# Optimization experiments

Hardware: AMD Instinct MI355X
Metric: run time of the kernel (lower is better)

Reference implementation:

```python
import jax, jax.numpy as jnp
from jax import lax
import numpy as np

B = 2; C = 128; H = 128; W = 128; NPIX = H * W
HTH = 184; HTW = 180; NBINS = HTH * HTW
NSPH = 16384; KHT = 8; KSPH = 16
N0, N1, N2 = 1024, 256, 64
K0, K1, K2 = 8, 8, 8
EPS = 1e-5


def setup_inputs() -> dict:
    key = jax.random.key(0)
    ks = jax.random.split(key, 24)
    f32 = jnp.float32
    inp = {}
    inp["image"] = jax.random.normal(ks[0], (B, C, H, W), f32)
    inp["bn_gamma"] = jnp.ones((C,), f32)
    inp["bn_beta"] = jnp.zeros((C,), f32)
    inp["ht_idx"] = jax.random.randint(ks[1], (NBINS, KHT), 0, NPIX, jnp.int32)
    inp["ht_w"] = jax.random.uniform(ks[2], (NBINS, KHT), f32)
    inp["w_htconv"] = jax.random.normal(ks[3], (3, 3, C, C), f32) / np.sqrt(9.0 * C)
    inp["htbn_gamma"] = jnp.ones((C,), f32)
    inp["htbn_beta"] = jnp.zeros((C,), f32)
    inp["sph_idx"] = jax.random.randint(ks[4], (NSPH, KSPH), 0, NBINS, jnp.int32)
    inp["sph_w"] = jax.random.uniform(ks[5], (NSPH, KSPH), f32)
    inp["w_sc"] = jax.random.normal(ks[6], (3, 64, C), f32) / np.sqrt(1.0 * C)
    inp["b_sc"] = jnp.zeros((3, 64), f32)
    inp["scbn_gamma"] = jnp.ones((3, 64), f32)
    inp["scbn_beta"] = jnp.zeros((3, 64), f32)
    inp["dgcn_w"] = jax.random.normal(ks[7], (3, 4, 128, 64), f32) / np.sqrt(128.0)
    inp["dgcn_b"] = jnp.zeros((3, 4, 64), f32)
    inp["dgcn_hw"] = jax.random.normal(ks[8], (3, 64), f32) / 8.0
    inp["dgcn_hb"] = jnp.zeros((3,), f32)
    inp["ind0"] = jax.random.randint(ks[9], (B, N0), 0, NSPH, jnp.int32)
    inp["ind1"] = jax.random.randint(ks[10], (B, 3, N1), 0, NSPH, jnp.int32)
    inp["ind2"] = jax.random.randint(ks[11], (B, 3, N2), 0, NSPH, jnp.int32)
    # kNN-style edges: structured centers (each node repeated k times), random neighbors
    c0 = jnp.tile(jnp.repeat(jnp.arange(N0, dtype=jnp.int32), K0)[None], (B, 1))
    inp["edge0"] = jnp.stack([c0, jax.random.randint(ks[12], (B, N0 * K0), 0, N0, jnp.int32)], 1)
    c1 = jnp.broadcast_to(jnp.repeat(jnp.arange(N1, dtype=jnp.int32), K1)[None, None], (B, 3, N1 * K1))
    inp["edge1"] = jnp.stack([c1, jax.random.randint(ks[13], (B, 3, N1 * K1), 0, N1, jnp.int32)], 2)
    c2 = jnp.broadcast_to(jnp.repeat(jnp.arange(N2, dtype=jnp.int32), K2)[None, None], (B, 3, N2 * K2))
    inp["edge2"] = jnp.stack([c2, jax.random.randint(ks[14], (B, 3, N2 * K2), 0, N2, jnp.int32)], 2)
    inp["target0"] = jax.random.randint(ks[15], (B, N0), 0, 2, jnp.int32)
    inp["target1"] = jax.random.randint(ks[16], (B * 3, N1), 0, 2, jnp.int32)
    inp["target2"] = jax.random.randint(ks[17], (B * 3, N2), 0, 2, jnp.int32)
    return inp


def _bn2d(x, g, b):
    m = x.mean((0, 2, 3), keepdims=True)
    v = x.var((0, 2, 3), keepdims=True)
    return g[None, :, None, None] * (x - m) * lax.rsqrt(v + EPS) + b[None, :, None, None]


def _sphere(x_htf, sph_idx, sph_w, ind):
    # x_htf: [B,C,NBINS]; ind: [B,S] -> weighted gather of HT bins per sphere node
    mi = sph_idx[ind]          # [B,S,K]
    mw = sph_w[ind]            # [B,S,K]
    g = jax.vmap(lambda xb, ib: xb[:, ib])(x_htf, mi)   # [B,C,S,K]
    return (g * mw[:, None]).sum(-1)                    # [B,C,S]


def _sconv(x, w, b, g, be):
    # 1x1 conv [B,C,S]->[B,64,S] + BN1d (batch stats) + ReLU
    y = jnp.einsum('oc,bcs->bos', w, x) + b[None, :, None]
    m = y.mean((0, 2), keepdims=True)
    v = y.var((0, 2), keepdims=True)
    return jax.nn.relu(g[None, :, None] * (y - m) * lax.rsqrt(v + EPS) + be[None, :, None])


def _dgcn(x, edge, ws, bs, hw, hb, n, k):
    # x: [Bg,n,64]; edge: [Bg,2,n*k] (row0=center, row1=neighbor); 4 EdgeConv layers
    for i in range(4):
        xc = jnp.take_along_axis(x, edge[:, 0, :, None], axis=1)   # [Bg,n*k,Cin]
        xn = jnp.take_along_axis(x, edge[:, 1, :, None], axis=1)
        h = jax.nn.relu(jnp.concatenate([xc, xn - xc], -1) @ ws[i] + bs[i])
        x = h.reshape(x.shape[0], n, k, -1).max(2)                 # max over neighbors
    return x @ hw + hb                                             # [Bg,n] logits


def _bce(logits, target):
    t = target.astype(logits.dtype)
    l = jnp.maximum(logits, 0.0) - logits * t + jnp.log1p(jnp.exp(-jnp.abs(logits)))
    pos = t > 0.5
    npos = jnp.maximum(pos.sum(), 1).astype(l.dtype)
    nneg = jnp.maximum((~pos).sum(), 1).astype(l.dtype)
    return jnp.where(pos, l, 0.0).sum() / npos, jnp.where(pos, 0.0, l).sum() / nneg


def _forward(image, bn_gamma, bn_beta, ht_idx, ht_w, w_htconv, htbn_gamma, htbn_beta,
             sph_idx, sph_w, w_sc, b_sc, scbn_gamma, scbn_beta,
             dgcn_w, dgcn_b, dgcn_hw, dgcn_hb,
             ind0, ind1, ind2, edge0, edge1, edge2, target0, target1, target2):
    x = jax.nn.relu(_bn2d(image, bn_gamma, bn_beta))
    xf = x.reshape(B, C, NPIX)
    # Hough voting: each HT bin accumulates KHT weighted pixels
    ht = (xf[:, :, ht_idx] * ht_w).sum(-1).reshape(B, C, HTH, HTW)
    hc = lax.conv_general_dilated(ht, w_htconv, (1, 1), 'SAME',
                                  dimension_numbers=('NCHW', 'HWIO', 'NCHW'))
    x_htf = jax.nn.relu(_bn2d(hc, htbn_gamma, htbn_beta)).reshape(B, C, NBINS)

    # scale 0
    x0 = _sconv(_sphere(x_htf, sph_idx, sph_w, ind0),
                w_sc[0], b_sc[0], scbn_gamma[0], scbn_beta[0]).transpose(0, 2, 1)
    x0 = _dgcn(x0, edge0, dgcn_w[0], dgcn_b[0], dgcn_hw[0], dgcn_hb[0], N0, K0)   # [B,N0]
    # scale 1 (3 vanishing-point branches folded into batch)
    x1 = _sconv(_sphere(x_htf, sph_idx, sph_w, ind1.reshape(B, -1)),
                w_sc[1], b_sc[1], scbn_gamma[1], scbn_beta[1]).transpose(0, 2, 1)
    x1 = _dgcn(x1.reshape(B * 3, N1, 64), edge1.reshape(B * 3, 2, N1 * K1),
               dgcn_w[1], dgcn_b[1], dgcn_hw[1], dgcn_hb[1], N1, K1)              # [B*3,N1]
    # scale 2
    x2 = _sconv(_sphere(x_htf, sph_idx, sph_w, ind2.reshape(B, -1)),
                w_sc[2], b_sc[2], scbn_gamma[2], scbn_beta[2]).transpose(0, 2, 1)
    x2 = _dgcn(x2.reshape(B * 3, N2, 64), edge2.reshape(B * 3, 2, N2 * K2),
               dgcn_w[2], dgcn_b[2], dgcn_hw[2], dgcn_hb[2], N2, K2)              # [B*3,N2]

    lp0, ln0 = _bce(x0, target0)
    lp1, ln1 = _bce(x1, target1)
    lp2, ln2 = _bce(x2, target2)
    losses = jnp.stack([lp0, ln0, lp1, ln1, lp2, ln2])
    preds = jnp.concatenate([jax.nn.sigmoid(x0).reshape(B, -1),
                             jax.nn.sigmoid(x1).reshape(B, -1),
                             jax.nn.sigmoid(x2).reshape(B, -1)], axis=1)
    return losses, preds


def reference(image, bn_gamma, bn_beta, ht_idx, ht_w, w_htconv, htbn_gamma, htbn_beta,
              sph_idx, sph_w, w_sc, b_sc, scbn_gamma, scbn_beta,
              dgcn_w, dgcn_b, dgcn_hw, dgcn_hb,
              ind0, ind1, ind2, edge0, edge1, edge2, target0, target1, target2):
    return _forward(image, bn_gamma, bn_beta, ht_idx, ht_w, w_htconv, htbn_gamma, htbn_beta,
                    sph_idx, sph_w, w_sc, b_sc, scbn_gamma, scbn_beta,
                    dgcn_w, dgcn_b, dgcn_hw, dgcn_hb,
                    ind0, ind1, ind2, edge0, edge1, edge2, target0, target1, target2)
```

## Files before the change

kernel.cpp:

```cpp
#include <hip/hip_runtime.h>
#include <math.h>

#define B_ 2
#define C_ 128
#define NPIX_ 16384
#define HTH_ 184
#define HTW_ 180
#define NBINS_ 33120
#define PH_ 186
#define PW_ 184
#define NPB_ 1984
#define TOTN_ 3968
#define EPS_ 1e-5f

#define ST_HC_SUM 0
#define ST_HC_SQ  128
#define ST_SC_SUM 256
#define ST_SC_SQ  448
#define ST_LOSS   640
#define ST_IMG_A  704
#define ST_IMG_D  832
#define ST_IMG_S1 1472
#define ST_IMG_S2 1600

typedef __attribute__((ext_vector_type(8))) short v8s;
typedef __attribute__((ext_vector_type(4))) float v4f;

__device__ inline unsigned short f2b(float f) {
  unsigned u = __builtin_bit_cast(unsigned, f);
  unsigned r = u + 0x7fffu + ((u >> 16) & 1u);
  return (unsigned short)(r >> 16);
}
__device__ inline float b2f(unsigned short u) {
  unsigned v = ((unsigned)u) << 16;
  return __builtin_bit_cast(float, v);
}

__global__ void kw_weights(const float* __restrict__ w, const float* __restrict__ dw,
                           unsigned short* __restrict__ wtb, unsigned short* __restrict__ dwb) {
  int i = blockIdx.x*256 + threadIdx.x;
  if (i < 147456) {
    int tap = i >> 14, z = i & 16383;
    int j = z & 7, lane = (z >> 3) & 63, nt = (z >> 9) & 7, kt = (z >> 12) & 3;
    int l = lane & 15, q = lane >> 4;
    int co = nt*16 + l, ci = kt*32 + q*8 + j;
    wtb[i] = f2b(w[(tap*C_ + ci)*C_ + co]);
  } else {
    int i2 = i - 147456;
    int sl = i2 >> 13, z = i2 & 8191;
    int j = z & 7, lane = (z >> 3) & 63, nt = (z >> 9) & 3, kt = (z >> 11) & 3;
    int l = lane & 15, q = lane >> 4;
    int co = nt*16 + l, cc = kt*32 + q*8 + j;
    dwb[i2] = f2b(dw[(sl*128 + cc)*64 + co]);
  }
}

__global__ void k1_img_stats(const float* __restrict__ img, float* __restrict__ st) {
  int c = blockIdx.x; int chunk = blockIdx.y; int tid = threadIdx.x;
  float s1 = 0.f, s2 = 0.f;
  for (int i = chunk*4096 + tid; i < (chunk+1)*4096; i += 256) {
    int b = i >> 14, p = i & (NPIX_-1);
    float v = img[((size_t)(b*C_ + c))*NPIX_ + p];
    s1 += v; s2 += v*v;
  }
  __shared__ float r1[256], r2[256];
  r1[tid] = s1; r2[tid] = s2; __syncthreads();
  for (int off = 128; off; off >>= 1) {
    if (tid < off) { r1[tid] += r1[tid+off]; r2[tid] += r2[tid+off]; }
    __syncthreads();
  }
  if (tid == 0) {
    atomicAdd(&st[ST_IMG_S1 + c], r1[0]);
    atomicAdd(&st[ST_IMG_S2 + c], r2[0]);
  }
}
__global__ void k1b_fin(const float* __restrict__ g, const float* __restrict__ be,
                        float* __restrict__ st) {
  int c = threadIdx.x;
  float n = (float)(B_*NPIX_);
  float m = st[ST_IMG_S1+c]/n;
  float var = st[ST_IMG_S2+c]/n - m*m;
  float a = g[c]*rsqrtf(var + EPS_);
  st[ST_IMG_A+c] = a; st[ST_IMG_D+c] = be[c] - a*m;
}

__global__ void k2_bnrelu_t(const float* __restrict__ img, const float* __restrict__ st,
                            unsigned short* __restrict__ xt) {
  __shared__ float tile[32*65];
  int p0 = blockIdx.x*64, c0 = blockIdx.y*32, b = blockIdx.z;
  int tid = threadIdx.x;
  for (int r = 0; r < 8; r++) {
    int flat = tid + r*256;
    int row = flat >> 6, col = flat & 63;
    int c = c0 + row;
    float v = img[((size_t)(b*C_ + c))*NPIX_ + p0 + col];
    tile[row*65 + col] = fmaxf(st[ST_IMG_A + c]*v + st[ST_IMG_D + c], 0.f);
  }
  __syncthreads();
  for (int r = 0; r < 4; r++) {
    int flat = (tid + r*256)*2;
    int pl = flat >> 5, cl = flat & 31;
    unsigned lo = f2b(tile[cl*65 + pl]);
    unsigned hi = f2b(tile[(cl+1)*65 + pl]);
    *(unsigned*)&xt[((size_t)b*NPIX_ + p0 + pl)*C_ + c0 + cl] = lo | (hi << 16);
  }
}

__global__ void k3_hough(const unsigned short* __restrict__ xt, const int* __restrict__ hidx,
                         const float* __restrict__ hwt, unsigned short* __restrict__ htb) {
  int tid = threadIdx.x;
  int bin = blockIdx.x*2 + (tid >> 7);
  int b = blockIdx.y;
  int c = tid & 127;
  float acc = 0.f;
  #pragma unroll
  for (int k = 0; k < 8; k++) {
    int p = hidx[bin*8 + k];
    float w = hwt[bin*8 + k];
    acc += w * b2f(xt[((size_t)b*NPIX_ + p)*C_ + c]);
  }
  int y = bin / HTW_, x = bin % HTW_;
  htb[(((size_t)(b*PH_ + y + 1))*PW_ + (x+1))*C_ + c] = f2b(acc);
}

__global__ __launch_bounds__(256) void k4_mfma(
    const unsigned short* __restrict__ htb, const unsigned short* __restrict__ wtb,
    unsigned short* __restrict__ hcb, float* __restrict__ st) {
  __shared__ unsigned short wl[16384];
  int tid = threadIdx.x;
  int w = tid >> 6, lane = tid & 63;
  int quad = lane >> 4, l16 = lane & 15;
  int ph = w & 1, ch = w >> 1;
  int b = blockIdx.y;
  int p0 = blockIdx.x*128 + ph*64;
  size_t ab[4];
  #pragma unroll
  for (int t = 0; t < 4; t++) {
    int px = p0 + t*16 + l16; if (px > NBINS_-1) px = NBINS_-1;
    int y = px / HTW_, x = px % HTW_;
    ab[t] = (((size_t)(b*PH_ + y))*PW_ + x)*C_ + quad*8;
  }
  v4f acc[4][4];
  #pragma unroll
  for (int t = 0; t < 4; t++)
    #pragma unroll
    for (int nt = 0; nt < 4; nt++) acc[t][nt] = (v4f){0,0,0,0};

  for (int tap = 0; tap < 9; tap++) {
    __syncthreads();
    const v8s* src = (const v8s*)(wtb + tap*16384);
    v8s* dst = (v8s*)wl;
    #pragma unroll
    for (int s = 0; s < 8; s++) dst[tid + s*256] = src[tid + s*256];
    __syncthreads();
    int dy = tap/3, dx = tap - dy*3;
    int toff = (dy*PW_ + dx)*C_;
    #pragma unroll
    for (int kt = 0; kt < 4; kt++) {
      v8s a[4];
      #pragma unroll
      for (int t = 0; t < 4; t++) a[t] = *(const v8s*)&htb[ab[t] + toff + kt*32];
      #pragma unroll
      for (int nt = 0; nt < 4; nt++) {
        v8s bf = *(const v8s*)&wl[((kt*8 + ch*4 + nt)*64 + lane)*8];
        #pragma unroll
        for (int t = 0; t < 4; t++)
          acc[t][nt] = __builtin_amdgcn_mfma_f32_16x16x32_bf16(a[t], bf, acc[t][nt], 0, 0, 0);
      }
    }
  }
  __syncthreads();
  float* red = (float*)wl;
  float s1[4] = {0,0,0,0}, s2[4] = {0,0,0,0};
  #pragma unroll
  for (int t = 0; t < 4; t++) {
    #pragma unroll
    for (int nt = 0; nt < 4; nt++) {
      int co = ch*64 + nt*16 + l16;
      #pragma unroll
      for (int reg = 0; reg < 4; reg++) {
        int po = p0 + t*16 + quad*4 + reg;
        if (po < NBINS_) {
          float v = acc[t][nt][reg];
          hcb[((size_t)b*NBINS_ + po)*C_ + co] = f2b(v);
          s1[nt] += v; s2[nt] += v*v;
        }
      }
    }
  }
  int slot = ph*4 + quad;
  #pragma unroll
  for (int nt = 0; nt < 4; nt++) red[(ch*64 + nt*16 + l16)*9 + slot] = s1[nt];
  __syncthreads();
  if (tid < 128) {
    float s = 0.f;
    #pragma unroll
    for (int k = 0; k < 8; k++) s += red[tid*9 + k];
    atomicAdd(&st[ST_HC_SUM + tid], s);
  }
  __syncthreads();
  #pragma unroll
  for (int nt = 0; nt < 4; nt++) red[(ch*64 + nt*16 + l16)*9 + slot] = s2[nt];
  __syncthreads();
  if (tid < 128) {
    float s = 0.f;
    #pragma unroll
    for (int k = 0; k < 8; k++) s += red[tid*9 + k];
    atomicAdd(&st[ST_HC_SQ + tid], s);
  }
}

__global__ void k6_sphere(const unsigned short* __restrict__ hcb, const float* __restrict__ st,
                          const float* __restrict__ g, const float* __restrict__ be,
                          const int* __restrict__ sph_idx, const float* __restrict__ sph_w,
                          const int* __restrict__ ind0, const int* __restrict__ ind1,
                          const int* __restrict__ ind2, float* __restrict__ out) {
  int gn = blockIdx.x; int c = threadIdx.x;
  int b = gn / NPB_, nb = gn % NPB_;
  int v;
  if (nb < 1024) v = ind0[b*1024 + nb];
  else if (nb < 1792) v = ind1[b*768 + nb - 1024];
  else v = ind2[b*192 + nb - 1792];
  float n = (float)(B_*NBINS_);
  float m = st[ST_HC_SUM + c]/n;
  float var = st[ST_HC_SQ + c]/n - m*m;
  float a = g[c]*rsqrtf(var + EPS_);
  float d = be[c] - a*m;
  float acc = 0.f;
  #pragma unroll
  for (int k = 0; k < 16; k++) {
    int mi = sph_idx[v*16 + k];
    float mw = sph_w[v*16 + k];
    float hv = b2f(hcb[((size_t)b*NBINS_ + mi)*C_ + c]);
    acc += mw * fmaxf(a*hv + d, 0.f);
  }
  out[(size_t)gn*C_ + c] = acc;
}

__global__ __launch_bounds__(256) void k7_sconv(
    const float* __restrict__ xin, const float* __restrict__ w_sc,
    const float* __restrict__ b_sc, float* __restrict__ y, float* __restrict__ st) {
  __shared__ float xs[32*128];
  __shared__ float wT[128*65];
  __shared__ float red[256];
  int tid = threadIdx.x;
  int gn0 = blockIdx.x * 32;
  int nb = gn0 % NPB_;
  int s = nb < 1024 ? 0 : (nb < 1792 ? 1 : 2);
  for (int r = 0; r < 16; r++) {
    int flat = tid + r*256;
    xs[flat] = xin[(size_t)gn0*C_ + flat];
  }
  for (int r = 0; r < 32; r++) {
    int flat = tid + r*256;
    int o = flat >> 7, cc = flat & 127;
    wT[cc*65 + o] = w_sc[(s*64 + o)*C_ + cc];
  }
  __syncthreads();
  int o = tid & 63, nl = tid >> 6;
  float bias = b_sc[s*64 + o];
  float acc[8];
  #pragma unroll
  for (int i = 0; i < 8; i++) acc[i] = bias;
  for (int cc = 0; cc < 128; cc++) {
    float wv = wT[cc*65 + o];
    #pragma unroll
    for (int i = 0; i < 8; i++)
      acc[i] += xs[(nl*8 + i)*128 + cc] * wv;
  }
  float s1 = 0.f, s2 = 0.f;
  #pragma unroll
  for (int i = 0; i < 8; i++) {
    y[(size_t)(gn0 + nl*8 + i)*64 + o] = acc[i];
    s1 += acc[i]; s2 += acc[i]*acc[i];
  }
  red[tid] = s1; __syncthreads();
  if (nl == 0) atomicAdd(&st[ST_SC_SUM + s*64 + o], red[o] + red[64+o] + red[128+o] + red[192+o]);
  __syncthreads();
  red[tid] = s2; __syncthreads();
  if (nl == 0) atomicAdd(&st[ST_SC_SQ + s*64 + o], red[o] + red[64+o] + red[128+o] + red[192+o]);
}

__global__ __launch_bounds__(256) void k10_dgcn(
    const void* __restrict__ xin_, unsigned short* __restrict__ xout,
    const int* __restrict__ edge0, const int* __restrict__ edge1, const int* __restrict__ edge2,
    const unsigned short* __restrict__ dwb, const float* __restrict__ db,
    const float* __restrict__ st, const float* __restrict__ scg, const float* __restrict__ scb,
    int layer, int usebn) {
  __shared__ unsigned short E[128*136];
  __shared__ float ash[64], dsh[64];
  int tid = threadIdx.x;
  int bid = blockIdx.x;
  int s, node_base, le_blk, span; const int* ec;
  if (bid < 128) {
    s = 0; int b = bid >> 6; node_base = b*NPB_; le_blk = (bid & 63)*128;
    span = 8192; ec = edge0 + b*2*8192;
  } else if (bid < 224) {
    int j = bid - 128; s = 1; int seg = j >> 4; int b = seg/3, vp = seg%3;
    node_base = b*NPB_ + 1024 + vp*256; le_blk = (j & 15)*128;
    span = 2048; ec = edge1 + ((b*3+vp)*2)*2048;
  } else {
    int j = bid - 224; s = 2; int seg = j >> 2; int b = seg/3, vp = seg%3;
    node_base = b*NPB_ + 1792 + vp*64; le_blk = (j & 3)*128;
    span = 512; ec = edge2 + ((b*3+vp)*2)*512;
  }
  const int* en = ec + span;
  if (usebn) {
    if (tid < 64) {
      float n = s==0 ? 2048.f : (s==1 ? 1536.f : 384.f);
      float m = st[ST_SC_SUM + s*64 + tid]/n;
      float var = st[ST_SC_SQ + s*64 + tid]/n - m*m;
      float a = scg[s*64 + tid]*rsqrtf(var + EPS_);
      ash[tid] = a; dsh[tid] = scb[s*64 + tid] - a*m;
    }
    __syncthreads();
  }
  {
    int r = tid >> 1, h = tid & 1;
    int e = le_blk + r;
    int ci = ec[e], ni = en[e];
    if (usebn) {
      const float* xc = (const float*)xin_ + (size_t)(node_base + ci)*64;
      const float* xn = (const float*)xin_ + (size_t)(node_base + ni)*64;
      #pragma unroll
      for (int c8 = 0; c8 < 64; c8 += 8) {
        v8s pk;
        #pragma unroll
        for (int j = 0; j < 8; j++) {
          int c = c8 + j;
          float vc = fmaxf(ash[c]*xc[c] + dsh[c], 0.f);
          float val = vc;
          if (h) val = fmaxf(ash[c]*xn[c] + dsh[c], 0.f) - vc;
          pk[j] = (short)f2b(val);
        }
        *(v8s*)&E[r*136 + h*64 + c8] = pk;
      }
    } else {
      const unsigned short* xc = (const unsigned short*)xin_ + (size_t)(node_base + ci)*64;
      const unsigned short* xn = (const unsigned short*)xin_ + (size_t)(node_base + ni)*64;
      #pragma unroll
      for (int c8 = 0; c8 < 64; c8 += 8) {
        v8s vc8 = *(const v8s*)&xc[c8];
        v8s pk = vc8;
        if (h) {
          v8s vn8 = *(const v8s*)&xn[c8];
          #pragma unroll
          for (int j = 0; j < 8; j++)
            pk[j] = (short)f2b(b2f((unsigned short)vn8[j]) - b2f((unsigned short)vc8[j]));
        }
        *(v8s*)&E[r*136 + h*64 + c8] = pk;
      }
    }
  }
  __syncthreads();
  int wave = tid >> 6, lane = tid & 63;
  int quad = lane >> 4, l16 = lane & 15;
  const unsigned short* wb = dwb + (size_t)(s*4 + layer)*8192;
  v4f acc[2][4];
  #pragma unroll
  for (int t = 0; t < 2; t++)
    #pragma unroll
    for (int nt = 0; nt < 4; nt++) acc[t][nt] = (v4f){0,0,0,0};
  #pragma unroll
  for (int kt = 0; kt < 4; kt++) {
    v8s a0 = *(const v8s*)&E[(wave*32 + l16)*136 + quad*8 + kt*32];
    v8s a1 = *(const v8s*)&E[(wave*32 + 16 + l16)*136 + quad*8 + kt*32];
    #pragma unroll
    for (int nt = 0; nt < 4; nt++) {
      v8s bf = *(const v8s*)&wb[((kt*4 + nt)*64 + lane)*8];
      acc[0][nt] = __builtin_amdgcn_mfma_f32_16x16x32_bf16(a0, bf, acc[0][nt], 0, 0, 0);
      acc[1][nt] = __builtin_amdgcn_mfma_f32_16x16x32_bf16(a1, bf, acc[1][nt], 0, 0, 0);
    }
  }
  int vb0 = le_blk/8 + wave*4;
  #pragma unroll
  for (int t = 0; t < 2; t++) {
    #pragma unroll
    for (int nt = 0; nt < 4; nt++) {
      float bias = db[(s*4 + layer)*64 + nt*16 + l16];
      float m = fmaxf(fmaxf(acc[t][nt][0], acc[t][nt][1]),
                      fmaxf(acc[t][nt][2], acc[t][nt][3]));
      m = fmaxf(m + bias, 0.f);
      float other = __shfl_xor(m, 16);
      m = fmaxf(m, other);
      if ((quad & 1) == 0) {
        int v = vb0 + t*2 + (quad >> 1);
        xout[(size_t)(node_base + v)*64 + nt*16 + l16] = f2b(m);
      }
    }
  }
}

__global__ __launch_bounds__(256) void k11_head(
    const unsigned short* __restrict__ x, const float* __restrict__ hw, const float* __restrict__ hb,
    const int* __restrict__ t0, const int* __restrict__ t1, const int* __restrict__ t2,
    float* __restrict__ out, float* __restrict__ st) {
  __shared__ float shw[192];
  int tid = threadIdx.x;
  if (tid < 192) shw[tid] = hw[tid];
  __syncthreads();
  int gn = blockIdx.x*256 + tid;
  bool valid = gn < TOTN_;
  int g = valid ? gn : TOTN_-1;
  int b = g / NPB_, nb = g % NPB_;
  int s, tg;
  if (nb < 1024) { s = 0; tg = t0[b*1024 + nb]; }
  else if (nb < 1792) { s = 1; int j = nb-1024; tg = t1[(b*3 + (j>>8))*256 + (j&255)]; }
  else { s = 2; int j = nb-1792; tg = t2[(b*3 + (j>>6))*64 + (j&63)]; }
  const unsigned short* row = x + (size_t)g*64;
  float logit = hb[s];
  #pragma unroll
  for (int c8 = 0; c8 < 64; c8 += 8) {
    v8s v = *(const v8s*)&row[c8];
    #pragma unroll
    for (int j = 0; j < 8; j++)
      logit += b2f((unsigned short)v[j]) * shw[s*64 + c8 + j];
  }
  if (valid) out[6 + gn] = 1.f / (1.f + expf(-logit));
  float tf = (float)tg;
  float l = fmaxf(logit, 0.f) - logit*tf + log1pf(expf(-fabsf(logit)));
  float sp = (valid && tg) ? l : 0.f;
  float sn = (valid && !tg) ? l : 0.f;
  float cp = (valid && tg) ? 1.f : 0.f;
  float cn = (valid && !tg) ? 1.f : 0.f;
  for (int off = 32; off; off >>= 1) {
    sp += __shfl_down(sp, off);
    sn += __shfl_down(sn, off);
    cp += __shfl_down(cp, off);
    cn += __shfl_down(cn, off);
  }
  if ((tid & 63) == 0) {
    atomicAdd(&st[ST_LOSS + s*4 + 0], sp);
    atomicAdd(&st[ST_LOSS + s*4 + 1], sn);
    atomicAdd(&st[ST_LOSS + s*4 + 2], cp);
    atomicAdd(&st[ST_LOSS + s*4 + 3], cn);
  }
}

__global__ void k12_fin(const float* __restrict__ st, float* __restrict__ out) {
  int i = threadIdx.x;
  if (i < 6) {
    int s = i >> 1; int pos = !(i & 1);
    float sum = st[ST_LOSS + s*4 + (pos ? 0 : 1)];
    float cnt = st[ST_LOSS + s*4 + (pos ? 2 : 3)];
    out[i] = sum / fmaxf(cnt, 1.f);
  }
}

extern "C" void kernel_launch(void* const* d_in, const int* in_sizes, int n_in,
                              void* d_out, int out_size, void* d_ws, size_t ws_size,
                              hipStream_t stream) {
  const float* image  = (const float*)d_in[0];
  const float* bn_g   = (const float*)d_in[1];
  const float* bn_b   = (const float*)d_in[2];
  const int*   ht_idx = (const int*)  d_in[3];
  const float* ht_w   = (const float*)d_in[4];
  const float* w_conv = (const float*)d_in[5];
  const float* htbn_g = (const float*)d_in[6];
  const float* htbn_b = (const float*)d_in[7];
  const int*   sph_idx= (const int*)  d_in[8];
  const float* sph_w  = (const float*)d_in[9];
  const float* w_sc   = (const float*)d_in[10];
  const float* b_sc   = (const float*)d_in[11];
  const float* scbn_g = (const float*)d_in[12];
  const float* scbn_b = (const float*)d_in[13];
  const float* dgcn_w = (const float*)d_in[14];
  const float* dgcn_b = (const float*)d_in[15];
  const float* dgcn_hw= (const float*)d_in[16];
  const float* dgcn_hb= (const float*)d_in[17];
  const int*   ind0   = (const int*)  d_in[18];
  const int*   ind1   = (const int*)  d_in[19];
  const int*   ind2   = (const int*)  d_in[20];
  const int*   edge0  = (const int*)  d_in[21];
  const int*   edge1  = (const int*)  d_in[22];
  const int*   edge2  = (const int*)  d_in[23];
  const int*   t0     = (const int*)  d_in[24];
  const int*   t1     = (const int*)  d_in[25];
  const int*   t2     = (const int*)  d_in[26];
  float* out = (float*)d_out;

  char* ws = (char*)d_ws;
  unsigned short* x_t   = (unsigned short*)(ws);
  unsigned short* htb   = (unsigned short*)(ws +  8388608);
  unsigned short* hcb   = (unsigned short*)(ws + 25911296);
  unsigned short* wtb   = (unsigned short*)(ws + 42868736);
  unsigned short* dwb   = (unsigned short*)(ws + 43163648);
  float*          sph_o = (float*)(ws + 43360256);
  float*          y_sc  = (float*)(ws + 45391872);
  unsigned short* xdgA  = (unsigned short*)(ws + 46407680);
  unsigned short* xdgB  = (unsigned short*)(ws + 46915584);
  float*          st    = (float*)(ws + 47423488);

  hipMemsetAsync(st, 0, 1728*sizeof(float), stream);
  hipMemsetAsync(htb, 0, 17522688, stream);
  kw_weights<<<960, 256, 0, stream>>>(w_conv, dgcn_w, wtb, dwb);
  k1_img_stats<<<dim3(128,8), 256, 0, stream>>>(image, st);
  k1b_fin<<<1, 128, 0, stream>>>(bn_g, bn_b, st);
  k2_bnrelu_t<<<dim3(256,4,2), 256, 0, stream>>>(image, st, x_t);
  k3_hough<<<dim3(NBINS_/2, B_), 256, 0, stream>>>(x_t, ht_idx, ht_w, htb);
  k4_mfma<<<dim3(259, 2), 256, 0, stream>>>(htb, wtb, hcb, st);
  k6_sphere<<<TOTN_, 128, 0, stream>>>(hcb, st, htbn_g, htbn_b, sph_idx, sph_w, ind0, ind1, ind2, sph_o);
  k7_sconv<<<TOTN_/32, 256, 0, stream>>>(sph_o, w_sc, b_sc, y_sc, st);
  k10_dgcn<<<248, 256, 0, stream>>>((const void*)y_sc, xdgA, edge0, edge1, edge2, dwb, dgcn_b, st, scbn_g, scbn_b, 0, 1);
  k10_dgcn<<<248, 256, 0, stream>>>((const void*)xdgA, xdgB, edge0, edge1, edge2, dwb, dgcn_b, st, scbn_g, scbn_b, 1, 0);
  k10_dgcn<<<248, 256, 0, stream>>>((const void*)xdgB, xdgA, edge0, edge1, edge2, dwb, dgcn_b, st, scbn_g, scbn_b, 2, 0);
  k10_dgcn<<<248, 256, 0, stream>>>((const void*)xdgA, xdgB, edge0, edge1, edge2, dwb, dgcn_b, st, scbn_g, scbn_b, 3, 0);
  k11_head<<<16, 256, 0, stream>>>(xdgB, dgcn_hw, dgcn_hb, t0, t1, t2, out, st);
  k12_fin<<<1, 64, 0, stream>>>(st, out);
}
```

Baseline: 288.5 us.

## Zero only conv padding border, pack bf16 pairs in gathers, read conv weights directly

The full 17.5 MB memset of the padded Hough buffer is replaced by a small kernel that zeroes only the one-pixel border. The Hough and sphere gather kernels now have each lane load two packed bf16 channels as one 32-bit word, with one wave per bin or node. The MFMA conv kernel stops staging each tap's weights in LDS behind two barriers and loads B fragments straight from global memory, relying on cache. Together these cut memory traffic and synchronization, at the cost of more global or L2 weight reads in the conv.

```diff
diff --git a/kernel.cpp b/kernel.cpp
--- a/kernel.cpp
+++ b/kernel.cpp
@@ -106,27 +106,43 @@
   }
 }
 
-__global__ void k3_hough(const unsigned short* __restrict__ xt, const int* __restrict__ hidx,
-                         const float* __restrict__ hwt, unsigned short* __restrict__ htb) {
-  int tid = threadIdx.x;
-  int bin = blockIdx.x*2 + (tid >> 7);
+__global__ void k3z_border(unsigned* __restrict__ htb2) {
+  int i = blockIdx.x*256 + threadIdx.x;
+  int d = i & 63;
+  int cell = i >> 6;
+  int b = cell / 1112, j = cell % 1112;
+  int y, x;
+  if (j < 184) { y = 0; x = j; }
+  else if (j < 368) { y = 185; x = j - 184; }
+  else { int c = j - 368; int xi = c / 186; y = c % 186; x = xi == 0 ? 0 : 180 + xi; }
+  htb2[((size_t)(b*PH_ + y)*PW_ + x)*64 + d] = 0u;
+}
+
+__global__ void k3_hough(const unsigned* __restrict__ xt2, const int* __restrict__ hidx,
+                         const float* __restrict__ hwt, unsigned* __restrict__ htb2) {
+  int tid = threadIdx.x;
+  int bin = blockIdx.x*4 + (tid >> 6);
   int b = blockIdx.y;
-  int c = tid & 127;
-  float acc = 0.f;
+  int lane = tid & 63;
+  const unsigned* base = xt2 + (size_t)b*NPIX_*64 + lane;
+  float acc0 = 0.f, acc1 = 0.f;
   #pragma unroll
   for (int k = 0; k < 8; k++) {
     int p = hidx[bin*8 + k];
     float w = hwt[bin*8 + k];
-    acc += w * b2f(xt[((size_t)b*NPIX_ + p)*C_ + c]);
-  }
-  int y = bin / HTW_, x = bin % HTW_;
-  htb[(((size_t)(b*PH_ + y + 1))*PW_ + (x+1))*C_ + c] = f2b(acc);
+    unsigned dv = base[(size_t)p*64];
+    acc0 += w * b2f((unsigned short)(dv & 0xffff));
+    acc1 += w * b2f((unsigned short)(dv >> 16));
+  }
+  int y = bin / HTW_, x = bin - y*HTW_;
+  unsigned lo = f2b(acc0), hi = f2b(acc1);
+  htb2[((size_t)(b*PH_ + y + 1)*PW_ + (x+1))*64 + lane] = lo | (hi << 16);
 }
 
 __global__ __launch_bounds__(256) void k4_mfma(
     const unsigned short* __restrict__ htb, const unsigned short* __restrict__ wtb,
     unsigned short* __restrict__ hcb, float* __restrict__ st) {
-  __shared__ unsigned short wl[16384];
+  __shared__ float red[1152];
   int tid = threadIdx.x;
   int w = tid >> 6, lane = tid & 63;
   int quad = lane >> 4, l16 = lane & 15;
@@ -146,13 +162,9 @@
     #pragma unroll
     for (int nt = 0; nt < 4; nt++) acc[t][nt] = (v4f){0,0,0,0};
 
+  const v8s* wbase = (const v8s*)wtb + lane;
+  #pragma unroll
   for (int tap = 0; tap < 9; tap++) {
-    __syncthreads();
-    const v8s* src = (const v8s*)(wtb + tap*16384);
-    v8s* dst = (v8s*)wl;
-    #pragma unroll
-    for (int s = 0; s < 8; s++) dst[tid + s*256] = src[tid + s*256];
-    __syncthreads();
     int dy = tap/3, dx = tap - dy*3;
     int toff = (dy*PW_ + dx)*C_;
     #pragma unroll
@@ -162,15 +174,13 @@
       for (int t = 0; t < 4; t++) a[t] = *(const v8s*)&htb[ab[t] + toff + kt*32];
       #pragma unroll
       for (int nt = 0; nt < 4; nt++) {
-        v8s bf = *(const v8s*)&wl[((kt*8 + ch*4 + nt)*64 + lane)*8];
+        v8s bf = wbase[(((tap*4 + kt)*8) + ch*4 + nt)*64];
         #pragma unroll
         for (int t = 0; t < 4; t++)
           acc[t][nt] = __builtin_amdgcn_mfma_f32_16x16x32_bf16(a[t], bf, acc[t][nt], 0, 0, 0);
       }
     }
   }
-  __syncthreads();
-  float* red = (float*)wl;
   float s1[4] = {0,0,0,0}, s2[4] = {0,0,0,0};
   #pragma unroll
   for (int t = 0; t < 4; t++) {
@@ -210,31 +220,36 @@
   }
 }
 
-__global__ void k6_sphere(const unsigned short* __restrict__ hcb, const float* __restrict__ st,
+__global__ void k6_sphere(const unsigned* __restrict__ hcb2, const float* __restrict__ st,
                           const float* __restrict__ g, const float* __restrict__ be,
                           const int* __restrict__ sph_idx, const float* __restrict__ sph_w,
                           const int* __restrict__ ind0, const int* __restrict__ ind1,
                           const int* __restrict__ ind2, float* __restrict__ out) {
-  int gn = blockIdx.x; int c = threadIdx.x;
+  int tid = threadIdx.x;
+  int gn = blockIdx.x*4 + (tid >> 6);
+  int lane = tid & 63;
   int b = gn / NPB_, nb = gn % NPB_;
   int v;
   if (nb < 1024) v = ind0[b*1024 + nb];
   else if (nb < 1792) v = ind1[b*768 + nb - 1024];
   else v = ind2[b*192 + nb - 1792];
+  int c0 = lane*2, c1 = c0 + 1;
   float n = (float)(B_*NBINS_);
-  float m = st[ST_HC_SUM + c]/n;
-  float var = st[ST_HC_SQ + c]/n - m*m;
-  float a = g[c]*rsqrtf(var + EPS_);
-  float d = be[c] - a*m;
-  float acc = 0.f;
+  float m0 = st[ST_HC_SUM + c0]/n, m1 = st[ST_HC_SUM + c1]/n;
+  float va0 = st[ST_HC_SQ + c0]/n - m0*m0, va1 = st[ST_HC_SQ + c1]/n - m1*m1;
+  float a0 = g[c0]*rsqrtf(va0 + EPS_), a1 = g[c1]*rsqrtf(va1 + EPS_);
+  float d0 = be[c0] - a0*m0, d1 = be[c1] - a1*m1;
+  const unsigned* base = hcb2 + (size_t)b*NBINS_*64 + lane;
+  float acc0 = 0.f, acc1 = 0.f;
   #pragma unroll
   for (int k = 0; k < 16; k++) {
     int mi = sph_idx[v*16 + k];
     float mw = sph_w[v*16 + k];
-    float hv = b2f(hcb[((size_t)b*NBINS_ + mi)*C_ + c]);
-    acc += mw * fmaxf(a*hv + d, 0.f);
-  }
-  out[(size_t)gn*C_ + c] = acc;
+    unsigned dv = base[(size_t)mi*64];
+    acc0 += mw * fmaxf(a0*b2f((unsigned short)(dv & 0xffff)) + d0, 0.f);
+    acc1 += mw * fmaxf(a1*b2f((unsigned short)(dv >> 16)) + d1, 0.f);
+  }
+  *(float2*)&out[(size_t)gn*C_ + c0] = make_float2(acc0, acc1);
 }
 
 __global__ __launch_bounds__(256) void k7_sconv(
@@ -492,14 +507,14 @@
   float*          st    = (float*)(ws + 47423488);
 
   hipMemsetAsync(st, 0, 1728*sizeof(float), stream);
-  hipMemsetAsync(htb, 0, 17522688, stream);
   kw_weights<<<960, 256, 0, stream>>>(w_conv, dgcn_w, wtb, dwb);
+  k3z_border<<<556, 256, 0, stream>>>((unsigned*)htb);
   k1_img_stats<<<dim3(128,8), 256, 0, stream>>>(image, st);
   k1b_fin<<<1, 128, 0, stream>>>(bn_g, bn_b, st);
   k2_bnrelu_t<<<dim3(256,4,2), 256, 0, stream>>>(image, st, x_t);
-  k3_hough<<<dim3(NBINS_/2, B_), 256, 0, stream>>>(x_t, ht_idx, ht_w, htb);
+  k3_hough<<<dim3(NBINS_/4, B_), 256, 0, stream>>>((const unsigned*)x_t, ht_idx, ht_w, (unsigned*)htb);
   k4_mfma<<<dim3(259, 2), 256, 0, stream>>>(htb, wtb, hcb, st);
-  k6_sphere<<<TOTN_, 128, 0, stream>>>(hcb, st, htbn_g, htbn_b, sph_idx, sph_w, ind0, ind1, ind2, sph_o);
+  k6_sphere<<<TOTN_/4, 256, 0, stream>>>((const unsigned*)hcb, st, htbn_g, htbn_b, sph_idx, sph_w, ind0, ind1, ind2, sph_o);
   k7_sconv<<<TOTN_/32, 256, 0, stream>>>(sph_o, w_sc, b_sc, y_sc, st);
   k10_dgcn<<<248, 256, 0, stream>>>((const void*)y_sc, xdgA, edge0, edge1, edge2, dwb, dgcn_b, st, scbn_g, scbn_b, 0, 1);
   k10_dgcn<<<248, 256, 0, stream>>>((const void*)xdgA, xdgB, edge0, edge1, edge2, dwb, dgcn_b, st, scbn_g, scbn_b, 1, 0);
```

Result: faster. 277.9 us (-3.7%).
